# Performance work log

Hardware: AMD Instinct MI355X
Metric: run time of the kernel (lower is better)

## Reference

```python
import jax, jax.numpy as jnp
import numpy as np

NU = 100000
NV = 100000
D = 128
R = 5          # num_support (rating levels)
O = 64         # output_dim // num_support
E = 640000     # edges per relation


def setup_inputs() -> dict:
    key = jax.random.key(0)
    ks = jax.random.split(key, 7)
    x_u = jax.random.normal(ks[0], (NU, D), dtype=jnp.float32)
    x_v = jax.random.normal(ks[1], (NV, D), dtype=jnp.float32)
    sup_rows = jax.random.randint(ks[2], (R, E), 0, NU, dtype=jnp.int32)
    sup_cols = jax.random.randint(ks[3], (R, E), 0, NV, dtype=jnp.int32)
    sup_vals = jax.random.uniform(ks[4], (R, E), dtype=jnp.float32)
    weights_u = jax.random.normal(ks[5], (R, D, O), dtype=jnp.float32)
    weights_v = jax.random.normal(ks[6], (R, D, O), dtype=jnp.float32)
    return {"x_u": x_u, "x_v": x_v, "sup_rows": sup_rows, "sup_cols": sup_cols,
            "sup_vals": sup_vals, "weights_u": weights_u, "weights_v": weights_v}


def _spmm(rows, cols, vals, feat, num_segments):
    # sparse [num_segments, n_src] @ feat [n_src, O] via gather + segment_sum
    return jax.ops.segment_sum(vals[:, None] * feat[cols], rows,
                               num_segments=num_segments)


def reference(x_u, x_v, sup_rows, sup_cols, sup_vals, weights_u, weights_v):
    # ordinal weight accumulation: wu_i = sum_{j<=i} weights_u[j]
    Wu = jnp.cumsum(weights_u, axis=0)  # [R, D, O]
    Wv = jnp.cumsum(weights_v, axis=0)  # [R, D, O]
    tmp_u = jnp.einsum('nd,rdo->rno', x_u, Wu)  # [R, NU, O]
    tmp_v = jnp.einsum('md,rdo->rmo', x_v, Wv)  # [R, NV, O]
    # z_u = sum_r support[r] @ tmp_v[r];  z_v = sum_r support[r]^T @ tmp_u[r]
    z_u = jax.vmap(lambda r, c, v, f: _spmm(r, c, v, f, NU))(
        sup_rows, sup_cols, sup_vals, tmp_v).sum(axis=0)
    z_v = jax.vmap(lambda r, c, v, f: _spmm(r, c, v, f, NV))(
        sup_cols, sup_rows, sup_vals, tmp_u).sum(axis=0)
    return jax.nn.relu(z_u), jax.nn.relu(z_v)
```

## Files before the change

kernel.cpp:

```cpp
#include <hip/hip_runtime.h>
#include <hip/hip_bf16.h>

#define R_SUP 5
#define D_IN 128
#define O_OUT 64
#define NBMAX 512
#define CHUNK 4096
#define FCAP 4608

typedef __attribute__((ext_vector_type(8))) short bf16x8;
typedef __attribute__((ext_vector_type(4))) float f32x4;

__device__ __forceinline__ unsigned short f2bf(float f) {
  union { float f; unsigned int u; } c; c.f = f;
  unsigned int u = c.u;
  return (unsigned short)((u + 0x7FFFu + ((u >> 16) & 1u)) >> 16);
}
__device__ __forceinline__ float bf2f(unsigned short h) {
  return __uint_as_float(((unsigned int)h) << 16);
}

__global__ __launch_bounds__(256) void cumsum_w(
    const float* __restrict__ wu, const float* __restrict__ wv,
    float* __restrict__ wcu, float* __restrict__ wcv,
    unsigned short* __restrict__ wtbu, unsigned short* __restrict__ wtbv) {
  int i = blockIdx.x * 256 + threadIdx.x;
  if (i >= D_IN * O_OUT) return;
  const int d = i >> 6;
  const int o = i & 63;
  float su = 0.f, sv = 0.f;
#pragma unroll
  for (int r = 0; r < R_SUP; ++r) {
    su += wu[r * D_IN * O_OUT + i];
    sv += wv[r * D_IN * O_OUT + i];
    wcu[r * D_IN * O_OUT + i] = su;
    wcv[r * D_IN * O_OUT + i] = sv;
    wtbu[((size_t)r * O_OUT + o) * D_IN + d] = f2bf(su);
    wtbv[((size_t)r * O_OUT + o) * D_IN + d] = f2bf(sv);
  }
}

__global__ __launch_bounds__(256) void zero_f32(float* __restrict__ p, int n4) {
  int i = blockIdx.x * 256 + threadIdx.x;
  int stride = gridDim.x * 256;
  float4 z = make_float4(0.f, 0.f, 0.f, 0.f);
  for (; i < n4; i += stride) ((float4*)p)[i] = z;
}

__global__ __launch_bounds__(256) void zero_i32(int* __restrict__ p, int n) {
  int i = blockIdx.x * 256 + threadIdx.x;
  int stride = gridDim.x * 256;
  for (; i < n; i += stride) p[i] = 0;
}

__global__ __launch_bounds__(256) void gemm5_mfma(
    const float* __restrict__ x,
    const unsigned short* __restrict__ wtb,
    unsigned short* __restrict__ tmp5, size_t strideR, int N) {
  __shared__ unsigned short st[64][72];
  const int tid = threadIdx.x;
  const int row0 = blockIdx.x * 64;
  const int wave = tid >> 6;
  const int lane = tid & 63;
  const int m = lane & 15;
  const int q = lane >> 4;
  const int o0 = wave * 16;

  bf16x8 a[4][4];
#pragma unroll
  for (int rt = 0; rt < 4; ++rt) {
    int row = row0 + rt * 16 + m;
    if (row >= N) row = N - 1;
    const float* px = x + (size_t)row * D_IN + q * 8;
#pragma unroll
    for (int k0 = 0; k0 < 4; ++k0) {
      float4 f0 = *(const float4*)(px + k0 * 32);
      float4 f1 = *(const float4*)(px + k0 * 32 + 4);
      bf16x8 t;
      t[0] = (short)f2bf(f0.x); t[1] = (short)f2bf(f0.y);
      t[2] = (short)f2bf(f0.z); t[3] = (short)f2bf(f0.w);
      t[4] = (short)f2bf(f1.x); t[5] = (short)f2bf(f1.y);
      t[6] = (short)f2bf(f1.z); t[7] = (short)f2bf(f1.w);
      a[rt][k0] = t;
    }
  }

  const int rr = tid >> 2;
  const int c0 = (tid & 3) * 16;

  for (int r = 0; r < R_SUP; ++r) {
    bf16x8 b[4];
    const unsigned short* pw =
        wtb + ((size_t)r * O_OUT + o0 + m) * D_IN + q * 8;
#pragma unroll
    for (int k0 = 0; k0 < 4; ++k0)
      b[k0] = *(const bf16x8*)(pw + k0 * 32);
#pragma unroll
    for (int rt = 0; rt < 4; ++rt) {
      f32x4 acc = {0.f, 0.f, 0.f, 0.f};
#pragma unroll
      for (int k0 = 0; k0 < 4; ++k0)
        acc = __builtin_amdgcn_mfma_f32_16x16x32_bf16(a[rt][k0], b[k0], acc,
                                                      0, 0, 0);
#pragma unroll
      for (int reg = 0; reg < 4; ++reg)
        st[rt * 16 + q * 4 + reg][o0 + m] = f2bf(acc[reg]);
    }
    __syncthreads();
    if (row0 + rr < N) {
      unsigned short* pz = tmp5 + (size_t)r * strideR + (size_t)row0 * O_OUT;
      *(int4*)(pz + rr * O_OUT + c0) = *(const int4*)&st[rr][c0];
      *(int4*)(pz + rr * O_OUT + c0 + 8) = *(const int4*)&st[rr][c0 + 8];
    }
    __syncthreads();
  }
}

__global__ __launch_bounds__(256) void coarse_hist(
    const int* __restrict__ rows, const int* __restrict__ cols,
    int* __restrict__ cnt_u, int* __restrict__ cnt_v, int nE5,
    int nbu, int nbv) {
  __shared__ int hu[NBMAX], hv[NBMAX];
  const int tid = threadIdx.x;
  for (int t = tid; t < NBMAX; t += 256) { hu[t] = 0; hv[t] = 0; }
  __syncthreads();
  const int n4 = nE5 >> 2;
  int i = blockIdx.x * 256 + tid;
  int stride = gridDim.x * 256;
  for (; i < n4; i += stride) {
    int4 rr = ((const int4*)rows)[i];
    int4 cc = ((const int4*)cols)[i];
    atomicAdd(&hu[rr.x >> 8], 1); atomicAdd(&hu[rr.y >> 8], 1);
    atomicAdd(&hu[rr.z >> 8], 1); atomicAdd(&hu[rr.w >> 8], 1);
    atomicAdd(&hv[cc.x >> 8], 1); atomicAdd(&hv[cc.y >> 8], 1);
    atomicAdd(&hv[cc.z >> 8], 1); atomicAdd(&hv[cc.w >> 8], 1);
  }
  for (i = (n4 << 2) + blockIdx.x * 256 + tid; i < nE5; i += stride) {
    atomicAdd(&hu[rows[i] >> 8], 1);
    atomicAdd(&hv[cols[i] >> 8], 1);
  }
  __syncthreads();
  for (int t = tid; t < nbu; t += 256) if (hu[t]) atomicAdd(&cnt_u[t], hu[t]);
  for (int t = tid; t < nbv; t += 256) if (hv[t]) atomicAdd(&cnt_v[t], hv[t]);
}

__global__ __launch_bounds__(512) void coarse_scan(
    int* __restrict__ cnt_u, int* __restrict__ cnt_v,
    int* __restrict__ cb_u, int* __restrict__ cb_v,
    int* __restrict__ gcur_u, int* __restrict__ gcur_v, int nbu, int nbv) {
  int* cnt = blockIdx.x ? cnt_v : cnt_u;
  int* cb  = blockIdx.x ? cb_v  : cb_u;
  int* gc  = blockIdx.x ? gcur_v : gcur_u;
  int nb   = blockIdx.x ? nbv   : nbu;
  __shared__ int sc[NBMAX];
  const int t = threadIdx.x;
  sc[t] = (t < nb) ? cnt[t] : 0;
  __syncthreads();
  for (int off = 1; off < NBMAX; off <<= 1) {
    int add = (t >= off) ? sc[t - off] : 0;
    __syncthreads();
    sc[t] += add;
    __syncthreads();
  }
  int excl = t ? sc[t - 1] : 0;
  if (t < nb) { cb[t] = excl; gc[t] = excl; }
  if (t == 0) cb[nb] = sc[NBMAX - 1];
}

__global__ __launch_bounds__(512) void coarse_scatter(
    const int* __restrict__ rows, const int* __restrict__ cols,
    const float* __restrict__ vals, int* __restrict__ gcur_u,
    int* __restrict__ gcur_v, int2* __restrict__ mid_u,
    int2* __restrict__ mid_v, int nE5, int E, int nbu, int nbv) {
  __shared__ int2 buf[CHUNK];
  __shared__ int h[NBMAX], sc[NBMAX], gb[NBMAX], cur[NBMAX];
  const int tid = threadIdx.x;
  const int dir = blockIdx.x & 1;
  const int base = (blockIdx.x >> 1) * CHUNK;
  const int end = min(base + CHUNK, nE5);
  const int E2 = 2 * E, E3 = 3 * E, E4 = 4 * E;

  const int* ids   = dir ? cols : rows;
  const int* other = dir ? rows : cols;
  int* gcur = dir ? gcur_v : gcur_u;
  int2* mid = dir ? mid_v : mid_u;
  const int nb = dir ? nbv : nbu;

  h[tid] = 0;
  __syncthreads();
  for (int i = base + tid; i < end; i += 512)
    atomicAdd(&h[ids[i] >> 8], 1);
  __syncthreads();
  sc[tid] = h[tid];
  __syncthreads();
  for (int off = 1; off < NBMAX; off <<= 1) {
    int add = (tid >= off) ? sc[tid - off] : 0;
    __syncthreads();
    sc[tid] += add;
    __syncthreads();
  }
  int excl = tid ? sc[tid - 1] : 0;
  cur[tid] = excl;
  if (tid < nb && h[tid]) gb[tid] = atomicAdd(&gcur[tid], h[tid]);
  __syncthreads();
  for (int i = base + tid; i < end; i += 512) {
    int id = ids[i];
    int src = other[i];
    int vb = __float_as_int(vals[i]);
    int r = (i >= E) + (i >= E2) + (i >= E3) + (i >= E4);
    int pos = atomicAdd(&cur[id >> 8], 1);
    buf[pos] = make_int2(((id & 255) << 20) | (r << 17) | src, vb);
  }
  __syncthreads();
  const int wv = tid >> 6;
  const int lane = tid & 63;
  for (int b = wv; b < nb; b += 8) {
    int s = b ? sc[b - 1] : 0;
    int e = sc[b];
    if (s == e) continue;
    int2* dst = mid + gb[b];
    for (int j = s + lane; j < e; j += 64) dst[j - s] = buf[j];
  }
}

__global__ __launch_bounds__(512) void spmm_sorted(
    const int2* __restrict__ mid, const int* __restrict__ cb,
    const unsigned short* __restrict__ tmp5, float* __restrict__ z,
    int Ndst, int strideR) {
  __shared__ int2 buf[FCAP];
  __shared__ int sc[256], cur[256];
  const int tid = threadIdx.x;
  const int b = blockIdx.x;
  const int s = cb[b];
  const int e = cb[b + 1];
  const int d0 = b * 256;
  const int gid = tid >> 4;
  const int lane = tid & 15;
  const unsigned short* tl = tmp5 + lane * 4;

  float4 acc[8];
#pragma unroll
  for (int k = 0; k < 8; ++k) acc[k] = make_float4(0.f, 0.f, 0.f, 0.f);

  for (int cs = s; cs < e; cs += FCAP) {
    const int ce = min(cs + FCAP, e);
    if (tid < 256) sc[tid] = 0;
    __syncthreads();
    for (int i = cs + tid; i < ce; i += 512)
      atomicAdd(&sc[(mid[i].x >> 20) & 255], 1);
    __syncthreads();
    for (int off = 1; off < 256; off <<= 1) {
      int add = (tid < 256 && tid >= off) ? sc[tid - off] : 0;
      __syncthreads();
      if (tid < 256) sc[tid] += add;
      __syncthreads();
    }
    if (tid < 256) cur[tid] = tid ? sc[tid - 1] : 0;
    __syncthreads();
    for (int i = cs + tid; i < ce; i += 512) {
      int2 pk = mid[i];
      int dl = (pk.x >> 20) & 255;
      int r = (pk.x >> 17) & 7;
      int src = pk.x & 0x1FFFF;
      int pos = atomicAdd(&cur[dl], 1);
      buf[pos] = make_int2(r * strideR + (src << 6), pk.y);
    }
    __syncthreads();
#pragma unroll
    for (int k = 0; k < 8; ++k) {
      const int dl = gid + (k << 5);
      int i = dl ? sc[dl - 1] : 0;
      const int re = sc[dl];
      float4 a = acc[k];
      for (; i + 8 <= re; i += 8) {
        int2 pk[8];
#pragma unroll
        for (int j = 0; j < 8; ++j) pk[j] = buf[i + j];
        ushort4 hh[8];
#pragma unroll
        for (int j = 0; j < 8; ++j)
          hh[j] = *(const ushort4*)(tl + (unsigned)pk[j].x);
#pragma unroll
        for (int j = 0; j < 8; ++j) {
          float v = __int_as_float(pk[j].y);
          a.x += v * bf2f(hh[j].x);
          a.y += v * bf2f(hh[j].y);
          a.z += v * bf2f(hh[j].z);
          a.w += v * bf2f(hh[j].w);
        }
      }
      for (; i < re; ++i) {
        int2 pk = buf[i];
        float v = __int_as_float(pk.y);
        ushort4 hh = *(const ushort4*)(tl + (unsigned)pk.x);
        a.x += v * bf2f(hh.x);
        a.y += v * bf2f(hh.y);
        a.z += v * bf2f(hh.z);
        a.w += v * bf2f(hh.w);
      }
      acc[k] = a;
    }
    __syncthreads();
  }
#pragma unroll
  for (int k = 0; k < 8; ++k) {
    int d = d0 + gid + (k << 5);
    if (d < Ndst) {
      float4 o;
      o.x = fmaxf(acc[k].x, 0.f);
      o.y = fmaxf(acc[k].y, 0.f);
      o.z = fmaxf(acc[k].z, 0.f);
      o.w = fmaxf(acc[k].w, 0.f);
      ((float4*)(z + (size_t)d * O_OUT))[lane] = o;
    }
  }
}

__global__ __launch_bounds__(256) void gemm64(
    const float* __restrict__ x, const float* __restrict__ w,
    float* __restrict__ out, int N) {
  __shared__ float sXT[D_IN][68];
  __shared__ float sW[D_IN][O_OUT];
  const int tid = threadIdx.x;
  const int row0 = blockIdx.x * 64;
  for (int i = tid; i < 2048; i += 256) {
    int d = i >> 4;
    int o4 = i & 15;
    ((float4*)&sW[d][0])[o4] = ((const float4*)w)[i];
  }
  for (int i = tid; i < 2048; i += 256) {
    int rl = i >> 5;
    int d4 = i & 31;
    int row = row0 + rl;
    float4 xv = make_float4(0.f, 0.f, 0.f, 0.f);
    if (row < N) xv = ((const float4*)x)[(size_t)row * 32 + d4];
    sXT[d4 * 4 + 0][rl] = xv.x;
    sXT[d4 * 4 + 1][rl] = xv.y;
    sXT[d4 * 4 + 2][rl] = xv.z;
    sXT[d4 * 4 + 3][rl] = xv.w;
  }
  __syncthreads();
  const int col4 = (tid & 15) * 4;
  const int row4 = (tid >> 4) * 4;
  float acc[4][4] = {};
#pragma unroll 8
  for (int d = 0; d < D_IN; ++d) {
    float4 xv = *(const float4*)&sXT[d][row4];
    float4 wv = *(const float4*)&sW[d][col4];
    acc[0][0] += xv.x * wv.x; acc[0][1] += xv.x * wv.y; acc[0][2] += xv.x * wv.z; acc[0][3] += xv.x * wv.w;
    acc[1][0] += xv.y * wv.x; acc[1][1] += xv.y * wv.y; acc[1][2] += xv.y * wv.z; acc[1][3] += xv.y * wv.w;
    acc[2][0] += xv.z * wv.x; acc[2][1] += xv.z * wv.y; acc[2][2] += xv.z * wv.z; acc[2][3] += xv.z * wv.w;
    acc[3][0] += xv.w * wv.x; acc[3][1] += xv.w * wv.y; acc[3][2] += xv.w * wv.z; acc[3][3] += xv.w * wv.w;
  }
#pragma unroll
  for (int i = 0; i < 4; ++i) {
    int row = row0 + row4 + i;
    if (row < N)
      *(float4*)&out[row * O_OUT + col4] =
          make_float4(acc[i][0], acc[i][1], acc[i][2], acc[i][3]);
  }
}

__global__ __launch_bounds__(256) void spmm_push(
    const int* __restrict__ dst, const int* __restrict__ src,
    const float* __restrict__ vals, const float* __restrict__ tmp,
    float* __restrict__ z, int E) {
  int t = blockIdx.x * 256 + threadIdx.x;
  int e = t >> 4;
  int lane = t & 15;
  if (e >= E) return;
  int d_ = dst[e];
  int s_ = src[e];
  float v = vals[e];
  float4 f = ((const float4*)tmp)[s_ * 16 + lane];
  float* zp = z + (size_t)d_ * O_OUT + lane * 4;
  atomicAdd(zp + 0, v * f.x);
  atomicAdd(zp + 1, v * f.y);
  atomicAdd(zp + 2, v * f.z);
  atomicAdd(zp + 3, v * f.w);
}

__global__ __launch_bounds__(256) void relu_f32(float* __restrict__ p, int n4) {
  int i = blockIdx.x * 256 + threadIdx.x;
  int stride = gridDim.x * 256;
  for (; i < n4; i += stride) {
    float4 v = ((float4*)p)[i];
    v.x = v.x > 0.f ? v.x : 0.f;
    v.y = v.y > 0.f ? v.y : 0.f;
    v.z = v.z > 0.f ? v.z : 0.f;
    v.w = v.w > 0.f ? v.w : 0.f;
    ((float4*)p)[i] = v;
  }
}

extern "C" void kernel_launch(void* const* d_in, const int* in_sizes, int n_in,
                              void* d_out, int out_size, void* d_ws, size_t ws_size,
                              hipStream_t stream) {
  const float* x_u      = (const float*)d_in[0];
  const float* x_v      = (const float*)d_in[1];
  const int*   sup_rows = (const int*)d_in[2];
  const int*   sup_cols = (const int*)d_in[3];
  const float* sup_vals = (const float*)d_in[4];
  const float* wu       = (const float*)d_in[5];
  const float* wv       = (const float*)d_in[6];

  const int NU = in_sizes[0] / D_IN;
  const int NV = in_sizes[1] / D_IN;
  const int E  = in_sizes[2] / R_SUP;
  const int Nmax = NU > NV ? NU : NV;
  const int nE5 = R_SUP * E;
  const int nbu = (NU + 255) / 256;
  const int nbv = (NV + 255) / 256;
  const int nbmax = nbu > nbv ? nbu : nbv;

  float* out = (float*)d_out;
  float* z_u = out;
  float* z_v = out + (size_t)NU * O_OUT;

  const int WDO = R_SUP * D_IN * O_OUT;
  const size_t strideR = (size_t)Nmax * O_OUT;
  const size_t bpad = (size_t)nbmax + 16;

  const size_t mid_bytes = (((size_t)nE5 * 8) + 255) & ~(size_t)255;

  const size_t needR = 2 * mid_bytes + strideR * R_SUP * 2 +
                       (size_t)2 * WDO * 4 + (size_t)2 * WDO * 2 +
                       6 * bpad * 4 + 512;

  if (ws_size >= needR && nbmax <= NBMAX && Nmax < (1 << 17)) {
    char* base = (char*)d_ws;
    int2* mid_u = (int2*)base;
    int2* mid_v = (int2*)(base + mid_bytes);
    unsigned short* tmp5 = (unsigned short*)(base + 2 * mid_bytes);
    float* wcu = (float*)(tmp5 + strideR * R_SUP);
    float* wcv = wcu + WDO;
    unsigned short* wtbu = (unsigned short*)(wcv + WDO);
    unsigned short* wtbv = wtbu + WDO;
    int* cnt_u = (int*)(wtbv + WDO);
    int* cnt_v = cnt_u + bpad;
    int* cb_u  = cnt_v + bpad;
    int* cb_v  = cb_u + bpad;
    int* gcur_u = cb_v + bpad;
    int* gcur_v = gcur_u + bpad;

    cumsum_w<<<(D_IN * O_OUT + 255) / 256, 256, 0, stream>>>(
        wu, wv, wcu, wcv, wtbu, wtbv);
    zero_i32<<<(2 * (int)bpad + 255) / 256, 256, 0, stream>>>(cnt_u, 2 * (int)bpad);
    coarse_hist<<<512, 256, 0, stream>>>(sup_rows, sup_cols, cnt_u, cnt_v,
                                         nE5, nbu, nbv);
    coarse_scan<<<2, 512, 0, stream>>>(cnt_u, cnt_v, cb_u, cb_v, gcur_u,
                                       gcur_v, nbu, nbv);
    coarse_scatter<<<2 * ((nE5 + CHUNK - 1) / CHUNK), 512, 0, stream>>>(
        sup_rows, sup_cols, sup_vals, gcur_u, gcur_v, mid_u, mid_v, nE5, E,
        nbu, nbv);

    gemm5_mfma<<<(NV + 63) / 64, 256, 0, stream>>>(x_v, wtbv, tmp5, strideR, NV);
    spmm_sorted<<<nbu, 512, 0, stream>>>(mid_u, cb_u, tmp5, z_u, NU,
                                         (int)strideR);

    gemm5_mfma<<<(NU + 63) / 64, 256, 0, stream>>>(x_u, wtbu, tmp5, strideR, NU);
    spmm_sorted<<<nbv, 512, 0, stream>>>(mid_v, cb_v, tmp5, z_v, NV,
                                         (int)strideR);
  } else {
    float* wcu = (float*)d_ws;
    float* wcv = wcu + WDO;
    unsigned short* wtbu = (unsigned short*)(wcv + WDO);
    unsigned short* wtbv = wtbu + WDO;
    float* tmp = (float*)(wtbv + WDO);
    const int n4_out = out_size / 4;
    cumsum_w<<<(D_IN * O_OUT + 255) / 256, 256, 0, stream>>>(
        wu, wv, wcu, wcv, wtbu, wtbv);
    zero_f32<<<1024, 256, 0, stream>>>(out, n4_out);
    const int spmm_blocks = (E * 16 + 255) / 256;
    for (int r = 0; r < R_SUP; ++r) {
      const int* rws = sup_rows + (size_t)r * E;
      const int* cls = sup_cols + (size_t)r * E;
      const float* vls = sup_vals + (size_t)r * E;
      gemm64<<<(NV + 63) / 64, 256, 0, stream>>>(x_v, wcv + r * D_IN * O_OUT, tmp, NV);
      spmm_push<<<spmm_blocks, 256, 0, stream>>>(rws, cls, vls, tmp, z_u, E);
      gemm64<<<(NU + 63) / 64, 256, 0, stream>>>(x_u, wcu + r * D_IN * O_OUT, tmp, NU);
      spmm_push<<<spmm_blocks, 256, 0, stream>>>(cls, rws, vls, tmp, z_v, E);
    }
    relu_f32<<<1024, 256, 0, stream>>>(out, n4_out);
  }
}
```

Baseline: 495.3 us.

## Stage x tile through swizzled LDS, widen gather unroll, enlarge scatter chunks

The GEMM kernel now loads each 64-row x tile with coalesced row-contiguous reads, converts it to bf16 once into an XOR-swizzled LDS buffer, and reads MFMA A-fragments from LDS instead of doing strided global loads per lane. The SpMM gather loop gets a 16-wide unrolled pass ahead of the 8-wide one to keep more independent loads in flight. CHUNK and FCAP are doubled so each coarse-scatter/fine block handles more edges. The workspace offset after tmp5 is 256-byte aligned. Costs are 16 KB more LDS in the GEMM kernel, more registers in the gather loop, and larger shared buffers, all of which can lower occupancy.

```diff
diff --git a/kernel.cpp b/kernel.cpp
--- a/kernel.cpp
+++ b/kernel.cpp
@@ -5,8 +5,8 @@
 #define D_IN 128
 #define O_OUT 64
 #define NBMAX 512
-#define CHUNK 4096
-#define FCAP 4608
+#define CHUNK 8192
+#define FCAP 9216
 
 typedef __attribute__((ext_vector_type(8))) short bf16x8;
 typedef __attribute__((ext_vector_type(4))) float f32x4;
@@ -57,6 +57,7 @@
     const float* __restrict__ x,
     const unsigned short* __restrict__ wtb,
     unsigned short* __restrict__ tmp5, size_t strideR, int N) {
+  __shared__ unsigned short lx[64 * 128];
   __shared__ unsigned short st[64][72];
   const int tid = threadIdx.x;
   const int row0 = blockIdx.x * 64;
@@ -66,23 +67,35 @@
   const int q = lane >> 4;
   const int o0 = wave * 16;
 
+#pragma unroll
+  for (int it = 0; it < 4; ++it) {
+    int idx = it * 2048 + tid * 8;
+    int row = idx >> 7;
+    int col = idx & 127;
+    int grow = row0 + row;
+    if (grow >= N) grow = N - 1;
+    const float* px = x + (size_t)grow * D_IN + col;
+    float4 f0 = *(const float4*)px;
+    float4 f1 = *(const float4*)(px + 4);
+    int4 pk4;
+    pk4.x = (int)f2bf(f0.x) | ((int)f2bf(f0.y) << 16);
+    pk4.y = (int)f2bf(f0.z) | ((int)f2bf(f0.w) << 16);
+    pk4.z = (int)f2bf(f1.x) | ((int)f2bf(f1.y) << 16);
+    pk4.w = (int)f2bf(f1.z) | ((int)f2bf(f1.w) << 16);
+    int byte = row * 256 + ((col * 2) ^ ((row & 7) << 4));
+    *(int4*)((char*)lx + byte) = pk4;
+  }
+  __syncthreads();
+
   bf16x8 a[4][4];
 #pragma unroll
   for (int rt = 0; rt < 4; ++rt) {
-    int row = row0 + rt * 16 + m;
-    if (row >= N) row = N - 1;
-    const float* px = x + (size_t)row * D_IN + q * 8;
-#pragma unroll
-    for (int k0 = 0; k0 < 4; ++k0) {
-      float4 f0 = *(const float4*)(px + k0 * 32);
-      float4 f1 = *(const float4*)(px + k0 * 32 + 4);
-      bf16x8 t;
-      t[0] = (short)f2bf(f0.x); t[1] = (short)f2bf(f0.y);
-      t[2] = (short)f2bf(f0.z); t[3] = (short)f2bf(f0.w);
-      t[4] = (short)f2bf(f1.x); t[5] = (short)f2bf(f1.y);
-      t[6] = (short)f2bf(f1.z); t[7] = (short)f2bf(f1.w);
-      a[rt][k0] = t;
-    }
+    const int rbase = (rt * 16 + m) * 256;
+    const int sw = (m & 7) << 4;
+#pragma unroll
+    for (int k0 = 0; k0 < 4; ++k0)
+      a[rt][k0] =
+          *(const bf16x8*)((const char*)lx + rbase + ((q * 16 + k0 * 64) ^ sw));
   }
 
   const int rr = tid >> 2;
@@ -272,6 +285,23 @@
       int i = dl ? sc[dl - 1] : 0;
       const int re = sc[dl];
       float4 a = acc[k];
+      for (; i + 16 <= re; i += 16) {
+        int2 pk[16];
+#pragma unroll
+        for (int j = 0; j < 16; ++j) pk[j] = buf[i + j];
+        ushort4 hh[16];
+#pragma unroll
+        for (int j = 0; j < 16; ++j)
+          hh[j] = *(const ushort4*)(tl + (unsigned)pk[j].x);
+#pragma unroll
+        for (int j = 0; j < 16; ++j) {
+          float v = __int_as_float(pk[j].y);
+          a.x += v * bf2f(hh[j].x);
+          a.y += v * bf2f(hh[j].y);
+          a.z += v * bf2f(hh[j].z);
+          a.w += v * bf2f(hh[j].w);
+        }
+      }
       for (; i + 8 <= re; i += 8) {
         int2 pk[8];
 #pragma unroll
@@ -422,17 +452,17 @@
   const size_t bpad = (size_t)nbmax + 16;
 
   const size_t mid_bytes = (((size_t)nE5 * 8) + 255) & ~(size_t)255;
-
-  const size_t needR = 2 * mid_bytes + strideR * R_SUP * 2 +
-                       (size_t)2 * WDO * 4 + (size_t)2 * WDO * 2 +
-                       6 * bpad * 4 + 512;
+  const size_t t5_bytes = (strideR * R_SUP * 2 + 255) & ~(size_t)255;
+
+  const size_t needR = 2 * mid_bytes + t5_bytes + (size_t)2 * WDO * 4 +
+                       (size_t)2 * WDO * 2 + 6 * bpad * 4 + 512;
 
   if (ws_size >= needR && nbmax <= NBMAX && Nmax < (1 << 17)) {
     char* base = (char*)d_ws;
     int2* mid_u = (int2*)base;
     int2* mid_v = (int2*)(base + mid_bytes);
     unsigned short* tmp5 = (unsigned short*)(base + 2 * mid_bytes);
-    float* wcu = (float*)(tmp5 + strideR * R_SUP);
+    float* wcu = (float*)(base + 2 * mid_bytes + t5_bytes);
     float* wcv = wcu + WDO;
     unsigned short* wtbu = (unsigned short*)(wcv + WDO);
     unsigned short* wtbv = wtbu + WDO;
```

After: 446.1 us. 9.9% less time.
